# Performance work log

Hardware: AMD Instinct MI355X
Metric: run time of the kernel (lower is better)

## Reference

```python
import jax, jax.numpy as jnp
import numpy as np

B, S, D, H, I, OUT, L, M = 4, 896, 1024, 16, 4096, 4096, 2, 128
EPS = 1e-12

def _ln(x, g, b):
    mu = jnp.mean(x, -1, keepdims=True)
    var = jnp.mean((x - mu) ** 2, -1, keepdims=True)
    return (x - mu) * jax.lax.rsqrt(var + EPS) * g + b

def _attn(x, Wq, bq, Wk, bk, Wv, bv, Wo, bo, g, b):
    Bb, T, Dd = x.shape
    Dh = Dd // H
    q = (x @ Wq + bq).reshape(Bb, T, H, Dh).transpose(0, 2, 1, 3)
    k = (x @ Wk + bk).reshape(Bb, T, H, Dh).transpose(0, 2, 1, 3)
    v = (x @ Wv + bv).reshape(Bb, T, H, Dh).transpose(0, 2, 1, 3)
    scores = jnp.einsum('bhqd,bhkd->bhqk', q, k) / jnp.sqrt(jnp.float32(Dh)).astype(x.dtype)
    p = jax.nn.softmax(scores, axis=-1)
    o = jnp.einsum('bhqk,bhkd->bhqd', p, v).transpose(0, 2, 1, 3).reshape(Bb, T, Dd)
    return _ln(o @ Wo + bo + x, g, b)  # Residual: dense -> (dropout=0) -> LN(h + input)

def _ffn(x, Wm, bm, Wr, br, g, b):
    inter = jax.nn.gelu(x @ Wm + bm, approximate=False)
    return _ln(inter @ Wr + br + x, g, b)

def setup_inputs() -> dict:
    key = jax.random.key(0)
    ks = jax.random.split(key, 24)
    s = 0.02
    d = {
        'hidden_states': jax.random.normal(ks[0], (B, S, D), jnp.float32),
        'mem_emb': jnp.zeros((M, D), jnp.float32),  # read_memory_emb init zeros
        'Wq': jax.random.normal(ks[1], (L, D, D), jnp.float32) * s,
        'bq': jnp.zeros((L, D), jnp.float32),
        'Wk': jax.random.normal(ks[2], (L, D, D), jnp.float32) * s,
        'bk': jnp.zeros((L, D), jnp.float32),
        'Wv': jax.random.normal(ks[3], (L, D, D), jnp.float32) * s,
        'bv': jnp.zeros((L, D), jnp.float32),
        'Wo': jax.random.normal(ks[4], (L, D, D), jnp.float32) * s,
        'bo': jnp.zeros((L, D), jnp.float32),
        'ln1_g': jnp.ones((L, D), jnp.float32),
        'ln1_b': jnp.zeros((L, D), jnp.float32),
        'Wm': jax.random.normal(ks[5], (L, D, I), jnp.float32) * s,
        'bm': jnp.zeros((L, I), jnp.float32),
        'Wr': jax.random.normal(ks[6], (L, I, D), jnp.float32) * s,
        'br': jnp.zeros((L, D), jnp.float32),
        'ln2_g': jnp.ones((L, D), jnp.float32),
        'ln2_b': jnp.zeros((L, D), jnp.float32),
        'Wp': jax.random.normal(ks[7], (D, OUT), jnp.float32) * s,
        'bp': jnp.zeros((OUT,), jnp.float32),
    }
    return d

def reference(hidden_states, mem_emb, Wq, bq, Wk, bk, Wv, bv, Wo, bo, ln1_g, ln1_b,
              Wm, bm, Wr, br, ln2_g, ln2_b, Wp, bp):
    Bb = hidden_states.shape[0]
    read_mem = jnp.broadcast_to(mem_emb[None], (Bb, M, D))
    x = jnp.concatenate([read_mem, hidden_states], axis=1)  # pack [b, m+s, d]
    for l in range(L):
        x = _attn(x, Wq[l], bq[l], Wk[l], bk[l], Wv[l], bv[l], Wo[l], bo[l], ln1_g[l], ln1_b[l])
        x = _ffn(x, Wm[l], bm[l], Wr[l], br[l], ln2_g[l], ln2_b[l])
    read_out = x[:, :M]
    out = jax.nn.gelu(x[:, M:] @ Wp + bp, approximate=False)
    return (out, read_out)
```

## Files before the change

kernel.cpp:

```cpp
#include <hip/hip_runtime.h>
#include <math.h>

#define B_    4
#define S_    896
#define D_    1024
#define H_    16
#define I_    4096
#define OUT_  4096
#define L_    2
#define M_    128
#define T_    1024
#define NROW  4096
#define DH    64

typedef unsigned short u16;
typedef unsigned int   u32;
typedef float  f32x4  __attribute__((ext_vector_type(4)));
typedef float  f32x16 __attribute__((ext_vector_type(16)));
typedef __bf16 bf16x8 __attribute__((ext_vector_type(8)));
typedef u16    u16x2  __attribute__((ext_vector_type(2)));
typedef u16    u16x4  __attribute__((ext_vector_type(4)));

typedef __attribute__((address_space(1))) const void gvoid;
typedef __attribute__((address_space(3))) void       lvoid;

__device__ __forceinline__ u16 f2bf(float f) {
  u32 u = __builtin_bit_cast(u32, f);
  u = (u + 0x7fffu + ((u >> 16) & 1u)) >> 16;
  return (u16)u;
}
__device__ __forceinline__ float geluf(float v) {
  return 0.5f * v * (1.0f + erff(v * 0.70710678118654752f));
}
__device__ __forceinline__ void gld16(const void* g, void* l) {
  __builtin_amdgcn_global_load_lds((gvoid*)g, (lvoid*)l, 16, 0, 0);
}

__global__ __launch_bounds__(256) void build_x(const float* __restrict__ hs,
                                               const float* __restrict__ mem,
                                               float* __restrict__ xf,
                                               u16* __restrict__ xb) {
  const long i  = (long)blockIdx.x * 256 + threadIdx.x;
  const int row = (int)(i >> 8);
  const int c4  = (int)(i & 255);
  const int bb  = row >> 10, t = row & 1023;
  f32x4 v;
  if (t < M_) v = ((const f32x4*)(mem + (long)t * D_))[c4];
  else        v = ((const f32x4*)(hs + (long)(bb * S_ + (t - M_)) * D_))[c4];
  ((f32x4*)xf)[i] = v;
  u16x4 ob;
  #pragma unroll
  for (int c = 0; c < 4; c++) ob[c] = f2bf(v[c]);
  ((u16x4*)xb)[i] = ob;
}

__global__ __launch_bounds__(256) void wtrans(const float* __restrict__ W,
                                              u16* __restrict__ WT, int K, int N) {
  __shared__ float t[32][33];
  const int n0 = blockIdx.x * 32, k0 = blockIdx.y * 32;
  const int tx = threadIdx.x, ty = threadIdx.y;
  #pragma unroll
  for (int r = 0; r < 32; r += 8)
    t[ty + r][tx] = W[(long)(k0 + ty + r) * N + n0 + tx];
  __syncthreads();
  #pragma unroll
  for (int r = 0; r < 32; r += 8)
    WT[(long)(n0 + ty + r) * K + k0 + tx] = f2bf(t[tx][ty + r]);
}

__global__ __launch_bounds__(256) void ln_k(const float* __restrict__ y,
                                            const float* __restrict__ ga,
                                            const float* __restrict__ be,
                                            float* __restrict__ xf,
                                            u16* __restrict__ xb) {
  const int row = blockIdx.x, tid = threadIdx.x;
  const f32x4 v = ((const f32x4*)(y + (long)row * D_))[tid];
  float s  = v[0] + v[1] + v[2] + v[3];
  float ss = v[0]*v[0] + v[1]*v[1] + v[2]*v[2] + v[3]*v[3];
  #pragma unroll
  for (int m = 1; m < 64; m <<= 1) { s += __shfl_xor(s, m); ss += __shfl_xor(ss, m); }
  __shared__ float sm[8];
  if ((tid & 63) == 0) { sm[tid >> 6] = s; sm[4 + (tid >> 6)] = ss; }
  __syncthreads();
  s  = sm[0] + sm[1] + sm[2] + sm[3];
  ss = sm[4] + sm[5] + sm[6] + sm[7];
  const float mu  = s * (1.0f / D_);
  const float var = ss * (1.0f / D_) - mu * mu;
  const float rs  = rsqrtf(var + 1e-12f);
  const f32x4 gg = ((const f32x4*)ga)[tid];
  const f32x4 bb = ((const f32x4*)be)[tid];
  f32x4 o; u16x4 ob;
  #pragma unroll
  for (int c = 0; c < 4; c++) { o[c] = (v[c] - mu) * rs * gg[c] + bb[c]; ob[c] = f2bf(o[c]); }
  ((f32x4*)(xf + (long)row * D_))[tid] = o;
  ((u16x4*)(xb + (long)row * D_))[tid] = ob;
}

__global__ __launch_bounds__(256) void copy_ro(const float* __restrict__ xf,
                                               float* __restrict__ dst) {
  const long i  = (long)blockIdx.x * 256 + threadIdx.x;
  const int row = (int)(i >> 8);
  const int c4  = (int)(i & 255);
  const int bb  = row >> 7, t = row & 127;
  f32x4 v = ((const f32x4*)(xf + (long)(bb * T_ + t) * D_))[c4];
  ((f32x4*)dst)[i] = v;
}

template <int EPI, int RMAP>
__global__ __launch_bounds__(256) void gemm_bt(const u16* __restrict__ A,
                                               const u16* __restrict__ BT,
                                               const float* __restrict__ bias0,
                                               const float* __restrict__ bias1,
                                               const float* __restrict__ bias2,
                                               const float* __restrict__ resid,
                                               float* __restrict__ of,
                                               u16* __restrict__ ob0,
                                               u16* __restrict__ ob1,
                                               u16* __restrict__ ob2,
                                               int M, int N, int K) {
  __shared__ u16 As[128 * 32];
  __shared__ u16 Bs[128 * 32];
  const int tid = threadIdx.x;
  const int l   = tid & 63;
  const int w   = tid >> 6;
  const int r16 = l & 15;
  const int g   = l >> 4;
  const int bm = blockIdx.x, bn = blockIdx.y;

  const int srow0 = w * 16 + (l >> 2);
  const int srow1 = srow0 + 64;
  const int scol  = (l & 3) * 8;
  long ar0 = (long)bm * 128 + srow0;
  long ar1 = (long)bm * 128 + srow1;
  if (RMAP == 1) {
    int R0 = (int)ar0, R1 = (int)ar1;
    ar0 = (long)(R0 / 896) * 1024 + 128 + (R0 % 896);
    ar1 = (long)(R1 / 896) * 1024 + 128 + (R1 % 896);
  }
  const u16* Ag0 = A + ar0 * K + scol;
  const u16* Ag1 = A + ar1 * K + scol;
  const u16* Bg0 = BT + ((long)bn * 128 + srow0) * K + scol;
  const u16* Bg1 = BT + ((long)bn * 128 + srow1) * K + scol;
  u16* AsD0 = As + w * 512; u16* AsD1 = As + (w + 4) * 512;
  u16* BsD0 = Bs + w * 512; u16* BsD1 = Bs + (w + 4) * 512;

  const int wm = w >> 1, wn = w & 1;
  const int aro = (wm * 64 + r16) * 32 + g * 8;
  const int bro = (wn * 64 + r16) * 32 + g * 8;

  f32x4 acc[4][4];
  #pragma unroll
  for (int i = 0; i < 4; i++)
    #pragma unroll
    for (int j = 0; j < 4; j++) acc[i][j] = (f32x4){0.f, 0.f, 0.f, 0.f};

  for (int k0 = 0; k0 < K; k0 += 32) {
    gld16(Ag0 + k0, AsD0);
    gld16(Ag1 + k0, AsD1);
    gld16(Bg0 + k0, BsD0);
    gld16(Bg1 + k0, BsD1);
    __syncthreads();
    bf16x8 af[4], bfr[4];
    #pragma unroll
    for (int i = 0; i < 4; i++) af[i]  = *(const bf16x8*)&As[aro + i * 512];
    #pragma unroll
    for (int j = 0; j < 4; j++) bfr[j] = *(const bf16x8*)&Bs[bro + j * 512];
    #pragma unroll
    for (int i = 0; i < 4; i++)
      #pragma unroll
      for (int j = 0; j < 4; j++)
        acc[i][j] = __builtin_amdgcn_mfma_f32_16x16x32_bf16(af[i], bfr[j], acc[i][j], 0, 0, 0);
    __syncthreads();
  }

  #pragma unroll
  for (int i = 0; i < 4; i++) {
    const int grow0 = bm * 128 + wm * 64 + i * 16 + g * 4;
    #pragma unroll
    for (int j = 0; j < 4; j++) {
      const int gcol = bn * 128 + wn * 64 + j * 16 + r16;
      f32x4 v = acc[i][j];
      if (EPI == 0) {
        const int bb = grow0 >> 10, t0 = grow0 & 1023;
        if (gcol < 1024) {
          const float bi = bias0[gcol];
          const int h = gcol >> 6, d = gcol & 63;
          u16* dst = ob0 + ((long)(bb * H_ + h) * T_) * DH + d;
          #pragma unroll
          for (int rr = 0; rr < 4; rr++) dst[(long)(t0 + rr) * DH] = f2bf((v[rr] + bi) * 0.125f);
        } else if (gcol < 2048) {
          const int c = gcol - 1024;
          const float bi = bias1[c];
          const int h = c >> 6, d = c & 63;
          u16* dst = ob1 + ((long)(bb * H_ + h) * T_) * DH + d;
          #pragma unroll
          for (int rr = 0; rr < 4; rr++) dst[(long)(t0 + rr) * DH] = f2bf(v[rr] + bi);
        } else {
          const int c = gcol - 2048;
          const float bi = bias2[c];
          const int h = c >> 6, d = c & 63;
          u16x4 pk;
          #pragma unroll
          for (int rr = 0; rr < 4; rr++) pk[rr] = f2bf(v[rr] + bi);
          *(u16x4*)(ob2 + ((long)(bb * H_ + h) * DH + d) * T_ + t0) = pk;
        }
      } else if (EPI == 1) {
        const float bi = bias0[gcol];
        #pragma unroll
        for (int rr = 0; rr < 4; rr++) {
          const long idx = (long)(grow0 + rr) * N + gcol;
          of[idx] = v[rr] + bi + resid[idx];
        }
      } else if (EPI == 2) {
        const float bi = bias0[gcol];
        #pragma unroll
        for (int rr = 0; rr < 4; rr++)
          ob0[(long)(grow0 + rr) * N + gcol] = f2bf(geluf(v[rr] + bi));
      } else {
        const float bi = bias0[gcol];
        #pragma unroll
        for (int rr = 0; rr < 4; rr++)
          of[(long)(grow0 + rr) * N + gcol] = geluf(v[rr] + bi);
      }
    }
  }
}

__global__ __launch_bounds__(256) void attn_k(const u16* __restrict__ qB,
                                              const u16* __restrict__ kB,
                                              const u16* __restrict__ vT,
                                              u16* __restrict__ ctx) {
  const int l   = threadIdx.x & 63, w = threadIdx.x >> 6;
  const int q31 = l & 31, hl = l >> 5;
  const int bh  = blockIdx.y, bb = bh >> 4, h = bh & 15;
  const int qbase = (blockIdx.x * 4 + w) * 32;
  const u16* qh = qB + (long)bh * T_ * DH;
  const u16* kh = kB + (long)bh * T_ * DH;
  const u16* vh = vT + (long)bh * DH * T_;

  bf16x8 qf[4];
  #pragma unroll
  for (int d0 = 0; d0 < 4; d0++)
    qf[d0] = *(const bf16x8*)&qh[(qbase + q31) * DH + d0 * 16 + hl * 8];

  f32x16 ot0, ot1;
  #pragma unroll
  for (int i = 0; i < 16; i++) { ot0[i] = 0.f; ot1[i] = 0.f; }
  float m = -1e30f, lsum = 0.f;

  for (int kb0 = 0; kb0 < T_; kb0 += 32) {
    bf16x8 vf0a = *(const bf16x8*)&vh[q31 * T_ + kb0 + hl * 8];
    bf16x8 vf0b = *(const bf16x8*)&vh[q31 * T_ + kb0 + 16 + hl * 8];
    bf16x8 vf1a = *(const bf16x8*)&vh[(32 + q31) * T_ + kb0 + hl * 8];
    bf16x8 vf1b = *(const bf16x8*)&vh[(32 + q31) * T_ + kb0 + 16 + hl * 8];

    f32x16 st;
    #pragma unroll
    for (int i = 0; i < 16; i++) st[i] = 0.f;
    #pragma unroll
    for (int d0 = 0; d0 < 4; d0++) {
      bf16x8 kf = *(const bf16x8*)&kh[(kb0 + q31) * DH + d0 * 16 + hl * 8];
      st = __builtin_amdgcn_mfma_f32_32x32x16_bf16(kf, qf[d0], st, 0, 0, 0);
    }

    float x0 = fmaxf(st[0], st[1]),   x1 = fmaxf(st[2], st[3]);
    float x2 = fmaxf(st[4], st[5]),   x3 = fmaxf(st[6], st[7]);
    float x4 = fmaxf(st[8], st[9]),   x5 = fmaxf(st[10], st[11]);
    float x6 = fmaxf(st[12], st[13]), x7 = fmaxf(st[14], st[15]);
    float pm = fmaxf(fmaxf(fmaxf(x0, x1), fmaxf(x2, x3)),
                     fmaxf(fmaxf(x4, x5), fmaxf(x6, x7)));
    {
      float a = pm, b = pm;
      asm("v_permlane32_swap_b32 %0, %1" : "+v"(a), "+v"(b));
      pm = fmaxf(a, b);
    }

    if (!__all(pm <= m + 8.0f)) {
      const float nm = fmaxf(m, pm);
      const float sc = __expf(m - nm);
      m = nm;
      lsum *= sc;
      #pragma unroll
      for (int i = 0; i < 16; i++) { ot0[i] *= sc; ot1[i] *= sc; }
    }

    float p[16], sum = 0.f;
    #pragma unroll
    for (int i = 0; i < 16; i++) { p[i] = __expf(st[i] - m); sum += p[i]; }
    {
      float a = sum, b = sum;
      asm("v_permlane32_swap_b32 %0, %1" : "+v"(a), "+v"(b));
      sum = a + b;
    }
    lsum += sum;

    u32 pk[8];
    #pragma unroll
    for (int i = 0; i < 8; i++)
      asm("v_cvt_pk_bf16_f32 %0, %1, %2" : "=v"(pk[i]) : "v"(p[2 * i]), "v"(p[2 * i + 1]));
    asm("v_permlane32_swap_b32 %0, %1" : "+v"(pk[0]), "+v"(pk[2]));
    asm("v_permlane32_swap_b32 %0, %1" : "+v"(pk[1]), "+v"(pk[3]));
    asm("v_permlane32_swap_b32 %0, %1" : "+v"(pk[4]), "+v"(pk[6]));
    asm("v_permlane32_swap_b32 %0, %1" : "+v"(pk[5]), "+v"(pk[7]));
    union { u32 u[4]; bf16x8 v; } f1, f2;
    f1.u[0] = pk[0]; f1.u[1] = pk[1]; f1.u[2] = pk[2]; f1.u[3] = pk[3];
    f2.u[0] = pk[4]; f2.u[1] = pk[5]; f2.u[2] = pk[6]; f2.u[3] = pk[7];

    ot0 = __builtin_amdgcn_mfma_f32_32x32x16_bf16(vf0a, f1.v, ot0, 0, 0, 0);
    ot0 = __builtin_amdgcn_mfma_f32_32x32x16_bf16(vf0b, f2.v, ot0, 0, 0, 0);
    ot1 = __builtin_amdgcn_mfma_f32_32x32x16_bf16(vf1a, f1.v, ot1, 0, 0, 0);
    ot1 = __builtin_amdgcn_mfma_f32_32x32x16_bf16(vf1b, f2.v, ot1, 0, 0, 0);
  }

  const float inv = 1.0f / lsum;
  u16* dst = ctx + ((long)(bb * T_ + qbase + q31)) * D_ + h * DH;
  #pragma unroll
  for (int rg = 0; rg < 4; rg++) {
    u16x4 o0, o1;
    #pragma unroll
    for (int r = 0; r < 4; r++) {
      o0[r] = f2bf(ot0[rg * 4 + r] * inv);
      o1[r] = f2bf(ot1[rg * 4 + r] * inv);
    }
    const int d0 = rg * 8 + hl * 4;
    *(u16x4*)(dst + d0) = o0;
    *(u16x4*)(dst + 32 + d0) = o1;
  }
}

extern "C" void kernel_launch(void* const* d_in, const int* in_sizes, int n_in,
                              void* d_out, int out_size, void* d_ws, size_t ws_size,
                              hipStream_t stream) {
  const float* hs  = (const float*)d_in[0];
  const float* mem = (const float*)d_in[1];
  const float* Wq  = (const float*)d_in[2];
  const float* bq  = (const float*)d_in[3];
  const float* Wk  = (const float*)d_in[4];
  const float* bk  = (const float*)d_in[5];
  const float* Wv  = (const float*)d_in[6];
  const float* bv  = (const float*)d_in[7];
  const float* Wo  = (const float*)d_in[8];
  const float* bo  = (const float*)d_in[9];
  const float* g1  = (const float*)d_in[10];
  const float* be1 = (const float*)d_in[11];
  const float* Wm  = (const float*)d_in[12];
  const float* bm  = (const float*)d_in[13];
  const float* Wr  = (const float*)d_in[14];
  const float* br  = (const float*)d_in[15];
  const float* g2  = (const float*)d_in[16];
  const float* be2 = (const float*)d_in[17];
  const float* Wp  = (const float*)d_in[18];
  const float* bp  = (const float*)d_in[19];
  float* out = (float*)d_out;

  char* ws = (char*)d_ws;
  float* xf  = (float*)(ws + 0);
  u16*   xb  = (u16*)  (ws + 16777216);
  float* yb  = (float*)(ws + 25165824);
  u16*   qb  = (u16*)  (ws + 41943040);
  u16*   kb2 = (u16*)  (ws + 50331648);
  u16*   vtb = (u16*)  (ws + 58720256);
  u16*   ctx = (u16*)  (ws + 67108864);
  u16*   ib  = qb;
  u16*   WTqkv = (u16*)(ws + 75497472);
  u16*   WTo   = (u16*)(ws + 88080384);
  u16*   WTm   = (u16*)(ws + 92274688);
  u16*   WTr   = (u16*)(ws + 109051904);
  u16*   WTp   = (u16*)(ws + 125829120);

  const dim3 blk(256);
  const dim3 tb(32, 8);

  build_x<<<dim3(4096), blk, 0, stream>>>(hs, mem, xf, xb);

  for (int l = 0; l < L_; l++) {
    wtrans<<<dim3(32, 32), tb, 0, stream>>>(Wq + (long)l * D_ * D_, WTqkv + (long)l * 3072 * 1024, 1024, 1024);
    wtrans<<<dim3(32, 32), tb, 0, stream>>>(Wk + (long)l * D_ * D_, WTqkv + (long)l * 3072 * 1024 + 1024 * 1024, 1024, 1024);
    wtrans<<<dim3(32, 32), tb, 0, stream>>>(Wv + (long)l * D_ * D_, WTqkv + (long)l * 3072 * 1024 + 2048 * 1024, 1024, 1024);
    wtrans<<<dim3(32, 32), tb, 0, stream>>>(Wo + (long)l * D_ * D_, WTo + (long)l * 1024 * 1024, 1024, 1024);
    wtrans<<<dim3(128, 32), tb, 0, stream>>>(Wm + (long)l * D_ * I_, WTm + (long)l * 4096 * 1024, 1024, 4096);
    wtrans<<<dim3(32, 128), tb, 0, stream>>>(Wr + (long)l * I_ * D_, WTr + (long)l * 4096 * 1024, 4096, 1024);
  }
  wtrans<<<dim3(128, 32), tb, 0, stream>>>(Wp, WTp, 1024, 4096);

  for (int l = 0; l < L_; l++) {
    gemm_bt<0, 0><<<dim3(32, 24), blk, 0, stream>>>(xb, WTqkv + (long)l * 3072 * 1024,
        bq + l * D_, bk + l * D_, bv + l * D_, nullptr,
        nullptr, qb, kb2, vtb, NROW, 3072, 1024);
    attn_k<<<dim3(8, 64), blk, 0, stream>>>(qb, kb2, vtb, ctx);
    gemm_bt<1, 0><<<dim3(32, 8), blk, 0, stream>>>(ctx, WTo + (long)l * 1024 * 1024,
        bo + l * D_, nullptr, nullptr, xf,
        yb, nullptr, nullptr, nullptr, NROW, 1024, 1024);
    ln_k<<<dim3(4096), blk, 0, stream>>>(yb, g1 + l * D_, be1 + l * D_, xf, xb);
    gemm_bt<2, 0><<<dim3(32, 32), blk, 0, stream>>>(xb, WTm + (long)l * 4096 * 1024,
        bm + l * I_, nullptr, nullptr, nullptr,
        nullptr, ib, nullptr, nullptr, NROW, 4096, 1024);
    gemm_bt<1, 0><<<dim3(32, 8), blk, 0, stream>>>(ib, WTr + (long)l * 4096 * 1024,
        br + l * D_, nullptr, nullptr, xf,
        yb, nullptr, nullptr, nullptr, NROW, 1024, 4096);
    ln_k<<<dim3(4096), blk, 0, stream>>>(yb, g2 + l * D_, be2 + l * D_, xf, xb);
  }

  gemm_bt<3, 1><<<dim3(28, 32), blk, 0, stream>>>(xb, WTp,
      bp, nullptr, nullptr, nullptr,
      out, nullptr, nullptr, nullptr, 3584, 4096, 1024);
  copy_ro<<<dim3(512), blk, 0, stream>>>(xf, out + 14680064);
}
```

Measured before the change: 913.2 us.

## Split-K the N=1024 GEMMs into three partials reduced inside the layernorm kernel

The output-projection and FFN-down GEMMs, which launched only 256 blocks, now use a 3-way split-K grid that writes fp32 partial sums to three buffers. A new layernorm kernel sums the partials, bias and residual before normalising. This raises the block count to improve CU occupancy on these GEMMs, at the cost of extra fp32 partial-buffer traffic. Weight transposes are also interleaved per layer into reused buffers to shrink the workspace.

```diff
diff --git a/kernel.cpp b/kernel.cpp
--- a/kernel.cpp
+++ b/kernel.cpp
@@ -68,13 +68,24 @@
     WT[(long)(n0 + ty + r) * K + k0 + tx] = f2bf(t[tx][ty + r]);
 }
 
-__global__ __launch_bounds__(256) void ln_k(const float* __restrict__ y,
-                                            const float* __restrict__ ga,
-                                            const float* __restrict__ be,
-                                            float* __restrict__ xf,
-                                            u16* __restrict__ xb) {
+__global__ __launch_bounds__(256) void lnred_k(const float* __restrict__ p0,
+                                               const float* __restrict__ p1,
+                                               const float* __restrict__ p2,
+                                               const float* __restrict__ bias,
+                                               const float* __restrict__ resid,
+                                               const float* __restrict__ ga,
+                                               const float* __restrict__ be,
+                                               float* __restrict__ xf,
+                                               u16* __restrict__ xb) {
   const int row = blockIdx.x, tid = threadIdx.x;
-  const f32x4 v = ((const f32x4*)(y + (long)row * D_))[tid];
+  const long ro = (long)row * D_;
+  f32x4 v = ((const f32x4*)(p0 + ro))[tid];
+  const f32x4 v1 = ((const f32x4*)(p1 + ro))[tid];
+  const f32x4 v2 = ((const f32x4*)(p2 + ro))[tid];
+  const f32x4 bi = ((const f32x4*)bias)[tid];
+  const f32x4 rs4 = ((const f32x4*)(resid + ro))[tid];
+  #pragma unroll
+  for (int c = 0; c < 4; c++) v[c] = v[c] + v1[c] + v2[c] + bi[c] + rs4[c];
   float s  = v[0] + v[1] + v[2] + v[3];
   float ss = v[0]*v[0] + v[1]*v[1] + v[2]*v[2] + v[3]*v[3];
   #pragma unroll
@@ -92,8 +103,8 @@
   f32x4 o; u16x4 ob;
   #pragma unroll
   for (int c = 0; c < 4; c++) { o[c] = (v[c] - mu) * rs * gg[c] + bb[c]; ob[c] = f2bf(o[c]); }
-  ((f32x4*)(xf + (long)row * D_))[tid] = o;
-  ((u16x4*)(xb + (long)row * D_))[tid] = ob;
+  ((f32x4*)(xf + ro))[tid] = o;
+  ((u16x4*)(xb + ro))[tid] = ob;
 }
 
 __global__ __launch_bounds__(256) void copy_ro(const float* __restrict__ xf,
@@ -112,12 +123,11 @@
                                                const float* __restrict__ bias0,
                                                const float* __restrict__ bias1,
                                                const float* __restrict__ bias2,
-                                               const float* __restrict__ resid,
                                                float* __restrict__ of,
                                                u16* __restrict__ ob0,
                                                u16* __restrict__ ob1,
                                                u16* __restrict__ ob2,
-                                               int M, int N, int K) {
+                                               int M, int N, int K, int KC) {
   __shared__ u16 As[128 * 32];
   __shared__ u16 Bs[128 * 32];
   const int tid = threadIdx.x;
@@ -126,6 +136,9 @@
   const int r16 = l & 15;
   const int g   = l >> 4;
   const int bm = blockIdx.x, bn = blockIdx.y;
+
+  const int kstart = (EPI == 4) ? blockIdx.z * KC : 0;
+  const int klen   = (EPI == 4) ? min(KC, K - kstart) : K;
 
   const int srow0 = w * 16 + (l >> 2);
   const int srow1 = srow0 + 64;
@@ -137,10 +150,10 @@
     ar0 = (long)(R0 / 896) * 1024 + 128 + (R0 % 896);
     ar1 = (long)(R1 / 896) * 1024 + 128 + (R1 % 896);
   }
-  const u16* Ag0 = A + ar0 * K + scol;
-  const u16* Ag1 = A + ar1 * K + scol;
-  const u16* Bg0 = BT + ((long)bn * 128 + srow0) * K + scol;
-  const u16* Bg1 = BT + ((long)bn * 128 + srow1) * K + scol;
+  const u16* Ag0 = A + ar0 * K + kstart + scol;
+  const u16* Ag1 = A + ar1 * K + kstart + scol;
+  const u16* Bg0 = BT + ((long)bn * 128 + srow0) * K + kstart + scol;
+  const u16* Bg1 = BT + ((long)bn * 128 + srow1) * K + kstart + scol;
   u16* AsD0 = As + w * 512; u16* AsD1 = As + (w + 4) * 512;
   u16* BsD0 = Bs + w * 512; u16* BsD1 = Bs + (w + 4) * 512;
 
@@ -154,7 +167,7 @@
     #pragma unroll
     for (int j = 0; j < 4; j++) acc[i][j] = (f32x4){0.f, 0.f, 0.f, 0.f};
 
-  for (int k0 = 0; k0 < K; k0 += 32) {
+  for (int k0 = 0; k0 < klen; k0 += 32) {
     gld16(Ag0 + k0, AsD0);
     gld16(Ag1 + k0, AsD1);
     gld16(Bg0 + k0, BsD0);
@@ -173,6 +186,7 @@
     __syncthreads();
   }
 
+  float* pof = (EPI == 4) ? of + (long)blockIdx.z * ((long)M * N) : of;
   #pragma unroll
   for (int i = 0; i < 4; i++) {
     const int grow0 = bm * 128 + wm * 64 + i * 16 + g * 4;
@@ -204,23 +218,20 @@
           for (int rr = 0; rr < 4; rr++) pk[rr] = f2bf(v[rr] + bi);
           *(u16x4*)(ob2 + ((long)(bb * H_ + h) * DH + d) * T_ + t0) = pk;
         }
-      } else if (EPI == 1) {
-        const float bi = bias0[gcol];
-        #pragma unroll
-        for (int rr = 0; rr < 4; rr++) {
-          const long idx = (long)(grow0 + rr) * N + gcol;
-          of[idx] = v[rr] + bi + resid[idx];
-        }
       } else if (EPI == 2) {
         const float bi = bias0[gcol];
         #pragma unroll
         for (int rr = 0; rr < 4; rr++)
           ob0[(long)(grow0 + rr) * N + gcol] = f2bf(geluf(v[rr] + bi));
-      } else {
+      } else if (EPI == 3) {
         const float bi = bias0[gcol];
         #pragma unroll
         for (int rr = 0; rr < 4; rr++)
           of[(long)(grow0 + rr) * N + gcol] = geluf(v[rr] + bi);
+      } else {
+        #pragma unroll
+        for (int rr = 0; rr < 4; rr++)
+          pof[(long)(grow0 + rr) * N + gcol] = v[rr];
       }
     }
   }
@@ -356,17 +367,19 @@
   char* ws = (char*)d_ws;
   float* xf  = (float*)(ws + 0);
   u16*   xb  = (u16*)  (ws + 16777216);
-  float* yb  = (float*)(ws + 25165824);
-  u16*   qb  = (u16*)  (ws + 41943040);
-  u16*   kb2 = (u16*)  (ws + 50331648);
-  u16*   vtb = (u16*)  (ws + 58720256);
-  u16*   ctx = (u16*)  (ws + 67108864);
+  float* p0  = (float*)(ws + 25165824);
+  float* p1  = (float*)(ws + 41943040);
+  float* p2  = (float*)(ws + 58720256);
+  u16*   qb  = (u16*)  (ws + 75497472);
+  u16*   kb2 = (u16*)  (ws + 83886080);
+  u16*   vtb = (u16*)  (ws + 92274688);
+  u16*   ctx = (u16*)  (ws + 100663296);
   u16*   ib  = qb;
-  u16*   WTqkv = (u16*)(ws + 75497472);
-  u16*   WTo   = (u16*)(ws + 88080384);
-  u16*   WTm   = (u16*)(ws + 92274688);
-  u16*   WTr   = (u16*)(ws + 109051904);
-  u16*   WTp   = (u16*)(ws + 125829120);
+  u16*   WTqkv = (u16*)(ws + 109051904);
+  u16*   WTo   = (u16*)(ws + 115343360);
+  u16*   WTm   = (u16*)(ws + 117440512);
+  u16*   WTr   = (u16*)(ws + 125829120);
+  u16*   WTp   = WTqkv;
 
   const dim3 blk(256);
   const dim3 tb(32, 8);
@@ -374,35 +387,35 @@
   build_x<<<dim3(4096), blk, 0, stream>>>(hs, mem, xf, xb);
 
   for (int l = 0; l < L_; l++) {
-    wtrans<<<dim3(32, 32), tb, 0, stream>>>(Wq + (long)l * D_ * D_, WTqkv + (long)l * 3072 * 1024, 1024, 1024);
-    wtrans<<<dim3(32, 32), tb, 0, stream>>>(Wk + (long)l * D_ * D_, WTqkv + (long)l * 3072 * 1024 + 1024 * 1024, 1024, 1024);
-    wtrans<<<dim3(32, 32), tb, 0, stream>>>(Wv + (long)l * D_ * D_, WTqkv + (long)l * 3072 * 1024 + 2048 * 1024, 1024, 1024);
-    wtrans<<<dim3(32, 32), tb, 0, stream>>>(Wo + (long)l * D_ * D_, WTo + (long)l * 1024 * 1024, 1024, 1024);
-    wtrans<<<dim3(128, 32), tb, 0, stream>>>(Wm + (long)l * D_ * I_, WTm + (long)l * 4096 * 1024, 1024, 4096);
-    wtrans<<<dim3(32, 128), tb, 0, stream>>>(Wr + (long)l * I_ * D_, WTr + (long)l * 4096 * 1024, 4096, 1024);
-  }
+    wtrans<<<dim3(32, 32), tb, 0, stream>>>(Wq + (long)l * D_ * D_, WTqkv, 1024, 1024);
+    wtrans<<<dim3(32, 32), tb, 0, stream>>>(Wk + (long)l * D_ * D_, WTqkv + 1024 * 1024, 1024, 1024);
+    wtrans<<<dim3(32, 32), tb, 0, stream>>>(Wv + (long)l * D_ * D_, WTqkv + 2048 * 1024, 1024, 1024);
+    wtrans<<<dim3(32, 32), tb, 0, stream>>>(Wo + (long)l * D_ * D_, WTo, 1024, 1024);
+    wtrans<<<dim3(128, 32), tb, 0, stream>>>(Wm + (long)l * D_ * I_, WTm, 1024, 4096);
+    wtrans<<<dim3(32, 128), tb, 0, stream>>>(Wr + (long)l * I_ * D_, WTr, 4096, 1024);
+
+    gemm_bt<0, 0><<<dim3(32, 24), blk, 0, stream>>>(xb, WTqkv,
+        bq + l * D_, bk + l * D_, bv + l * D_,
+        nullptr, qb, kb2, vtb, NROW, 3072, 1024, 0);
+    attn_k<<<dim3(8, 64), blk, 0, stream>>>(qb, kb2, vtb, ctx);
+    gemm_bt<4, 0><<<dim3(32, 8, 3), blk, 0, stream>>>(ctx, WTo,
+        nullptr, nullptr, nullptr,
+        p0, nullptr, nullptr, nullptr, NROW, 1024, 1024, 352);
+    lnred_k<<<dim3(4096), blk, 0, stream>>>(p0, p1, p2, bo + l * D_, xf,
+        g1 + l * D_, be1 + l * D_, xf, xb);
+    gemm_bt<2, 0><<<dim3(32, 32), blk, 0, stream>>>(xb, WTm,
+        bm + l * I_, nullptr, nullptr,
+        nullptr, ib, nullptr, nullptr, NROW, 4096, 1024, 0);
+    gemm_bt<4, 0><<<dim3(32, 8, 3), blk, 0, stream>>>(ib, WTr,
+        nullptr, nullptr, nullptr,
+        p0, nullptr, nullptr, nullptr, NROW, 1024, 4096, 1376);
+    lnred_k<<<dim3(4096), blk, 0, stream>>>(p0, p1, p2, br + l * D_, xf,
+        g2 + l * D_, be2 + l * D_, xf, xb);
+  }
+
   wtrans<<<dim3(128, 32), tb, 0, stream>>>(Wp, WTp, 1024, 4096);
-
-  for (int l = 0; l < L_; l++) {
-    gemm_bt<0, 0><<<dim3(32, 24), blk, 0, stream>>>(xb, WTqkv + (long)l * 3072 * 1024,
-        bq + l * D_, bk + l * D_, bv + l * D_, nullptr,
-        nullptr, qb, kb2, vtb, NROW, 3072, 1024);
-    attn_k<<<dim3(8, 64), blk, 0, stream>>>(qb, kb2, vtb, ctx);
-    gemm_bt<1, 0><<<dim3(32, 8), blk, 0, stream>>>(ctx, WTo + (long)l * 1024 * 1024,
-        bo + l * D_, nullptr, nullptr, xf,
-        yb, nullptr, nullptr, nullptr, NROW, 1024, 1024);
-    ln_k<<<dim3(4096), blk, 0, stream>>>(yb, g1 + l * D_, be1 + l * D_, xf, xb);
-    gemm_bt<2, 0><<<dim3(32, 32), blk, 0, stream>>>(xb, WTm + (long)l * 4096 * 1024,
-        bm + l * I_, nullptr, nullptr, nullptr,
-        nullptr, ib, nullptr, nullptr, NROW, 4096, 1024);
-    gemm_bt<1, 0><<<dim3(32, 8), blk, 0, stream>>>(ib, WTr + (long)l * 4096 * 1024,
-        br + l * D_, nullptr, nullptr, xf,
-        yb, nullptr, nullptr, nullptr, NROW, 1024, 4096);
-    ln_k<<<dim3(4096), blk, 0, stream>>>(yb, g2 + l * D_, be2 + l * D_, xf, xb);
-  }
-
   gemm_bt<3, 1><<<dim3(28, 32), blk, 0, stream>>>(xb, WTp,
-      bp, nullptr, nullptr, nullptr,
-      out, nullptr, nullptr, nullptr, 3584, 4096, 1024);
+      bp, nullptr, nullptr,
+      out, nullptr, nullptr, nullptr, 3584, 4096, 1024, 0);
   copy_ro<<<dim3(512), blk, 0, stream>>>(xf, out + 14680064);
 }
```

Result: faster. 844.6 us (-7.5%).
